# Optimization experiments

Hardware: AMD Instinct MI355X
Metric: run time of the kernel (lower is better)

The kernel has to match this reference:

```python
import jax, jax.numpy as jnp
import numpy as np
import math

DIM = 512      # vMF embedding dim
B = 512        # batch
K = 10         # sample_size
C = 8192       # num_classes
L = 0.7        # kappa_confidence
T_REJ = 32     # fixed rejection-sampling tries (acceptance ~0.7 per try)


def _vmf_logc(k, dim=DIM):
    # Approximate log normalizer from the paper (approximate_logc=True path).
    nm14 = (dim - 1) / 4.0
    nm12 = (dim - 1) / 2.0
    np12 = (dim + 1) / 2.0
    sqrtm = jnp.sqrt(nm12 * nm12 + k * k)
    sqrtp = jnp.sqrt(np12 * np12 + k * k)
    return nm14 * (jnp.log(nm12 + sqrtm) + jnp.log(nm12 + sqrtp)) - 0.5 * (sqrtm + sqrtp)


def _split(params):
    # params layout: [log_probs(1), means(DIM), hidden_ik(1)] (single component).
    means = params[..., 1:1 + DIM]
    hidden_ik = params[..., -1]
    mu = means / jnp.linalg.norm(means, axis=-1, keepdims=True)
    kappa = 1.0 / jnp.exp(hidden_ik)  # positive(x) = exp(x) parametrization
    return mu, kappa


def _vmf_sample(key, mu, kappa, n):
    # Wood's algorithm, vectorized over (b, n) with fixed-count rejection.
    b, d = mu.shape
    kap = kappa[:, None]  # (b,1)
    bb = (-2.0 * kap + jnp.sqrt(4.0 * kap * kap + (d - 1) ** 2)) / (d - 1)
    x0 = (1.0 - bb) / (1.0 + bb)
    cc = kap * x0 + (d - 1) * jnp.log(1.0 - x0 * x0)
    kz, ku, kv = jax.random.split(key, 3)
    z = jax.random.beta(kz, (d - 1) / 2.0, (d - 1) / 2.0, (T_REJ, b, n))
    w = (1.0 - (1.0 + bb) * z) / (1.0 - (1.0 - bb) * z)  # (T,b,n)
    u = jax.random.uniform(ku, (T_REJ, b, n), minval=1e-10)
    acc = kap * w + (d - 1) * jnp.log(1.0 - x0 * w) - cc >= jnp.log(u)
    idx = jnp.argmax(acc, axis=0)  # first accepted try
    w_sel = jnp.take_along_axis(w, idx[None], axis=0)[0]  # (b,n)
    v = jax.random.normal(kv, (b, n, d))
    v = v - jnp.einsum('bnd,bd->bn', v, mu)[..., None] * mu[:, None, :]
    v = v / jnp.linalg.norm(v, axis=-1, keepdims=True)
    sin_t = jnp.sqrt(jnp.clip(1.0 - w_sel * w_sel, 0.0))
    return w_sel[..., None] * mu[:, None, :] + sin_t[..., None] * v  # (b,n,d)


def setup_inputs() -> dict:
    key = jax.random.key(0)
    kp, kw, kl = jax.random.split(key, 3)
    # Input distribution parameters: random means, hidden_ik ~ log(1/kappa) with realistic kappa.
    parameters = jax.random.normal(kp, (B, DIM + 2), dtype=jnp.float32)
    kappa0 = L / (1.0 - L * L) * (DIM - 1) / math.sqrt(DIM)  # ~31
    parameters = parameters.at[:, -1].set(0.1 * parameters[:, -1] - math.log(kappa0))
    # Class weight, built exactly as in __init__ (non-deterministic target).
    means = jax.random.normal(kw, (C, DIM), dtype=jnp.float32) * (L / (1.0 - L * L) * (DIM - 1) / math.sqrt(DIM))
    norm = jnp.linalg.norm(means, axis=-1, keepdims=True)
    hidden_ik = jnp.log(1.0 / norm)  # ipositive = log
    weight = jnp.concatenate([jnp.zeros((C, 1), jnp.float32), means, hidden_ik], axis=-1)
    log_scale = jnp.asarray(2.773, dtype=jnp.float32)
    labels = jax.random.randint(kl, (B,), 0, C)
    return {"parameters": parameters, "weight": weight, "log_scale": log_scale, "labels": labels}


def reference(parameters, weight, log_scale, labels):
    scale = jnp.exp(log_scale)
    mu_x, kappa_x = _split(parameters)   # (b,d), (b,)
    mu_w, kappa_w = _split(weight)       # (c,d), (c,)
    sample = _vmf_sample(jax.random.key(42), mu_x, kappa_x, K)  # (b,K,d)
    sample = sample / jnp.linalg.norm(sample, axis=-1, keepdims=True)
    # logmls(b,k,c): samples have concentration k1=scale; since all means are unit,
    # ||k1*m1 + k2*m2|| = sqrt(k1^2 + k2^2 + 2*k1*k2*cos) -> single GEMM over d.
    cos = jnp.einsum('bkd,cd->bkc', sample, mu_w)
    k1 = scale
    k2 = kappa_w
    kk = jnp.sqrt(k1 * k1 + k2 * k2 + 2.0 * k1 * (k2 * cos))  # (b,K,c)
    logmls = _vmf_logc(k1) + _vmf_logc(k2)[None, None, :] - _vmf_logc(kk)
    neg_logden = jax.scipy.special.logsumexp(logmls, axis=2) - _vmf_logc(scale)  # (b,K)
    neg_lognum = scale * jnp.einsum('bd,bd->b', mu_x, mu_w[labels])
    losses = neg_logden.mean(axis=1) - neg_lognum  # (b,)
    b = parameters.shape[0]
    logits = jnp.zeros((b, C), parameters.dtype).at[jnp.arange(b), labels].set(-losses)
    return logits
```

## Files before the change

kernel.cpp:

```cpp
#include <hip/hip_runtime.h>
#include <stdint.h>

#define DIMD 512
#define BATCH 512
#define KSAMP 10
#define NCLS 8192
#define TREJ 32

typedef __bf16 bf16x8 __attribute__((ext_vector_type(8)));
typedef float f32x4 __attribute__((ext_vector_type(4)));

__device__ inline uint64_t sm64(uint64_t x) {
  x += 0x9E3779B97F4A7C15ull;
  x = (x ^ (x >> 30)) * 0xBF58476D1CE4E5B9ull;
  x = (x ^ (x >> 27)) * 0x94D049BB133111EBull;
  return x ^ (x >> 31);
}
__device__ inline float u01(uint32_t u) {
  return ((float)u + 0.5f) * 2.3283064365386963e-10f;
}
__device__ inline float normal_from(uint64_t r) {
  float u1 = u01((uint32_t)(r >> 32));
  float u2 = u01((uint32_t)r);
  return sqrtf(-2.0f * __logf(u1)) * __cosf(6.28318530718f * u2);
}
__device__ inline float gamma255(uint64_t& ctr) {
  const float dg = 255.1666667f;
  const float cg = 0.02086730f;
  for (int i = 0; i < 16; i++) {
    uint64_t r = sm64(ctr++);
    float x = normal_from(r);
    float t = fmaf(cg, x, 1.0f);
    if (t <= 0.0f) continue;
    float v3 = t * t * t;
    uint64_t r2 = sm64(ctr++);
    float u3 = u01((uint32_t)(r2 >> 32));
    if (__logf(u3) < 0.5f * x * x + dg * (1.0f - v3 + __logf(v3))) return dg * v3;
  }
  return dg;
}
__device__ inline float wave_sum(float v) {
  #pragma unroll
  for (int o = 32; o > 0; o >>= 1) v += __shfl_down(v, o, 64);
  return __shfl(v, 0, 64);
}
__device__ inline float vmf_logc(float k) {
  float k2 = k * k;
  float sm = sqrtf(65280.25f + k2);
  float sp = sqrtf(65792.25f + k2);
  return 127.75f * (logf(255.5f + sm) + logf(255.5f + sp)) - 0.5f * (sm + sp);
}
__device__ inline unsigned short f2bf(float f) {
  uint32_t u = __float_as_uint(f);
  uint32_t r = (u + 0x7FFFu + ((u >> 16) & 1u)) >> 16;
  return (unsigned short)r;
}
__device__ inline float bf2f(unsigned short s) {
  return __uint_as_float(((uint32_t)s) << 16);
}
__device__ inline void async16(const unsigned short* g, unsigned short* l) {
  __builtin_amdgcn_global_load_lds(
      (const __attribute__((address_space(1))) unsigned int*)g,
      (__attribute__((address_space(3))) unsigned int*)l, 16, 0, 0);
}

__global__ __launch_bounds__(256) void prep_w(const float* __restrict__ weight,
                                              const float* __restrict__ lscale,
                                              unsigned short* __restrict__ muWb,
                                              float4* __restrict__ cparams,
                                              float* __restrict__ rowsum,
                                              float4* __restrict__ out4) {
  __shared__ float red[4];
  int c = blockIdx.x, tid = threadIdx.x;
  if (tid < 128) out4[(size_t)c * 128 + tid] = make_float4(0.f, 0.f, 0.f, 0.f);
  if (c < 20) rowsum[c * 256 + tid] = 0.0f;

  const float* wr = weight + (size_t)c * (DIMD + 2) + 1;
  float v0 = wr[tid], v1 = wr[tid + 256];
  float s = wave_sum(v0 * v0 + v1 * v1);
  if ((tid & 63) == 0) red[tid >> 6] = s;
  __syncthreads();
  float tot = red[0] + red[1] + red[2] + red[3];
  float inv = rsqrtf(tot);
  muWb[(size_t)c * DIMD + tid]       = f2bf(v0 * inv);
  muWb[(size_t)c * DIMD + tid + 256] = f2bf(v1 * inv);
  if (tid == 0) {
    float hik = weight[(size_t)c * (DIMD + 2) + DIMD + 1];
    float kw = expf(-hik);
    float k1 = expf(lscale[0]);
    float lcw = vmf_logc(kw);
    float A2 = fmaf(k1, k1, kw * kw);
    float B2 = 2.0f * k1 * kw;
    const float X0 = 0.9238795f, X1 = 0.3826834f;
    float g0 = lcw - vmf_logc(sqrtf(fmaf(B2,  X0, A2)));
    float g1 = lcw - vmf_logc(sqrtf(fmaf(B2,  X1, A2)));
    float g2 = lcw - vmf_logc(sqrtf(fmaf(B2, -X1, A2)));
    float g3 = lcw - vmf_logc(sqrtf(fmaf(B2, -X0, A2)));
    float b0 = 0.25f * (g0 + g1 + g2 + g3);
    float b1 = 0.5f * (X0 * (g0 - g3) + X1 * (g1 - g2));
    float b2 = 0.5f * 0.7071068f * ((g0 + g3) - (g1 + g2));
    float b3 = 0.5f * (X1 * (g0 - g3) - X0 * (g1 - g2));
    const float L2E = 1.4426950409f;
    cparams[c] = make_float4((b0 - b2) * L2E, (b1 - 3.0f * b3) * L2E,
                             (2.0f * b2) * L2E, (4.0f * b3) * L2E);
  }
}

__global__ __launch_bounds__(256) void sample_kernel(const float* __restrict__ params,
                                                     unsigned short* __restrict__ Sb) {
  int wave = threadIdx.x >> 6, lane = threadIdx.x & 63;
  int row = blockIdx.x * 4 + wave;
  int b = row / KSAMP;
  const float* pr = params + (size_t)b * (DIMD + 2) + 1;

  float mu[8];
  float n2 = 0.0f;
  #pragma unroll
  for (int j = 0; j < 8; j++) { mu[j] = pr[j * 64 + lane]; n2 += mu[j] * mu[j]; }
  n2 = wave_sum(n2);
  float invn = rsqrtf(n2);
  #pragma unroll
  for (int j = 0; j < 8; j++) mu[j] *= invn;

  float kap = __expf(-pr[DIMD]);
  float bb = (-2.0f * kap + sqrtf(fmaf(4.0f * kap, kap, 511.0f * 511.0f))) / 511.0f;
  float x0 = (1.0f - bb) / (1.0f + bb);
  float cc = kap * x0 + 511.0f * __logf(1.0f - x0 * x0);

  uint64_t ctr = (((uint64_t)(row + 1)) << 32) | ((uint64_t)lane << 8);
  float g1 = gamma255(ctr);
  float g2 = gamma255(ctr);
  float z = g1 / (g1 + g2);
  float wt = (1.0f - (1.0f + bb) * z) / (1.0f - (1.0f - bb) * z);
  uint64_t r = sm64(ctr++);
  float u = u01((uint32_t)(r >> 32));
  float lhs = kap * wt + 511.0f * __logf(1.0f - x0 * wt) - cc;
  bool acc = (lane < TREJ) && (lhs >= __logf(fmaxf(u, 1e-10f)));
  uint64_t mask = __ballot(acc);
  int sel = mask ? (__ffsll((unsigned long long)mask) - 1) : 0;
  float w = __shfl(wt, sel, 64);

  uint64_t cbase = (((uint64_t)(row + 1)) << 32) | 0x40000000ull;
  float v[8];
  #pragma unroll
  for (int j = 0; j < 8; j++) v[j] = normal_from(sm64(cbase + (uint64_t)(j * 64 + lane)));
  float d = 0.0f;
  #pragma unroll
  for (int j = 0; j < 8; j++) d += v[j] * mu[j];
  d = wave_sum(d);
  float t2 = 0.0f;
  #pragma unroll
  for (int j = 0; j < 8; j++) { v[j] -= d * mu[j]; t2 += v[j] * v[j]; }
  t2 = wave_sum(t2);
  float ivt = rsqrtf(t2);
  float st = sqrtf(fmaxf(0.0f, 1.0f - w * w)) * ivt;
  float sv[8];
  float s2 = 0.0f;
  #pragma unroll
  for (int j = 0; j < 8; j++) { sv[j] = fmaf(st, v[j], w * mu[j]); s2 += sv[j] * sv[j]; }
  s2 = wave_sum(s2);
  float is = rsqrtf(s2);
  #pragma unroll
  for (int j = 0; j < 8; j++) Sb[(size_t)row * DIMD + j * 64 + lane] = f2bf(sv[j] * is);
}

__global__ __launch_bounds__(256, 2) void gemm_lse(const unsigned short* __restrict__ Sb,
                                                   const unsigned short* __restrict__ Wb,
                                                   const float4* __restrict__ cparams,
                                                   float* __restrict__ rowsum) {
  __shared__ __align__(16) unsigned short As[2][256 * 32];
  __shared__ __align__(16) unsigned short Bs[2][128 * 32];
  int tid = threadIdx.x;
  int lane = tid & 63, wave = tid >> 6;
  int tx = lane & 15, tz = lane >> 4;

  int id = blockIdx.x;
  int xcd = id & 7, lid = id >> 3;
  int c0 = (xcd * 8 + (lid & 7)) * 128;
  int r0 = (lid >> 3) * 256;

  int srow = (lane >> 2);
  int kg   = (lane & 3) ^ ((lane >> 3) & 3);
  int chA0 = wave * 4;
  int chB0 = wave * 2;

  f32x4 acc[4][8];
  #pragma unroll
  for (int i = 0; i < 4; i++)
    #pragma unroll
    for (int j = 0; j < 8; j++) acc[i][j] = (f32x4){0.f, 0.f, 0.f, 0.f};

  #pragma unroll
  for (int c = 0; c < 4; c++) {
    int ch = chA0 + c, rowi = ch * 16 + srow;
    async16(&Sb[(size_t)(r0 + rowi) * DIMD + kg * 8], &As[0][ch * 512]);
  }
  #pragma unroll
  for (int c = 0; c < 2; c++) {
    int ch = chB0 + c, rowi = ch * 16 + srow;
    async16(&Wb[(size_t)(c0 + rowi) * DIMD + kg * 8], &Bs[0][ch * 512]);
  }

  int p = 0;
  for (int kt = 0; kt < DIMD; kt += 32) {
    __syncthreads();
    if (kt + 32 < DIMD) {
      #pragma unroll
      for (int c = 0; c < 4; c++) {
        int ch = chA0 + c, rowi = ch * 16 + srow;
        async16(&Sb[(size_t)(r0 + rowi) * DIMD + kt + 32 + kg * 8], &As[p ^ 1][ch * 512]);
      }
      #pragma unroll
      for (int c = 0; c < 2; c++) {
        int ch = chB0 + c, rowi = ch * 16 + srow;
        async16(&Wb[(size_t)(c0 + rowi) * DIMD + kt + 32 + kg * 8], &Bs[p ^ 1][ch * 512]);
      }
    }
    bf16x8 af[4], bf[8];
    int sA = tz ^ ((tx >> 1) & 3);
    #pragma unroll
    for (int mi = 0; mi < 4; mi++) {
      int rA = wave * 64 + mi * 16 + tx;
      af[mi] = *(const bf16x8*)&As[p][rA * 32 + sA * 8];
    }
    #pragma unroll
    for (int ni = 0; ni < 8; ni++) {
      int rB = ni * 16 + tx;
      bf[ni] = *(const bf16x8*)&Bs[p][rB * 32 + sA * 8];
    }
    #pragma unroll
    for (int mi = 0; mi < 4; mi++)
      #pragma unroll
      for (int ni = 0; ni < 8; ni++)
        acc[mi][ni] = __builtin_amdgcn_mfma_f32_16x16x32_bf16(af[mi], bf[ni], acc[mi][ni], 0, 0, 0);
    p ^= 1;
  }

  float4 cp[8];
  #pragma unroll
  for (int ni = 0; ni < 8; ni++) cp[ni] = cparams[c0 + ni * 16 + tx];

  #pragma unroll
  for (int mi = 0; mi < 4; mi++) {
    #pragma unroll
    for (int reg = 0; reg < 4; reg++) {
      float s = 0.0f;
      #pragma unroll
      for (int ni = 0; ni < 8; ni++) {
        float cv = acc[mi][ni][reg];
        float g = fmaf(fmaf(fmaf(cp[ni].w, cv, cp[ni].z), cv, cp[ni].y), cv, cp[ni].x);
        s += exp2f(g);
      }
      #pragma unroll
      for (int o = 1; o < 16; o <<= 1) s += __shfl_xor(s, o, 64);
      if (tx == 0)
        atomicAdd(&rowsum[r0 + wave * 64 + mi * 16 + tz * 4 + reg], s);
    }
  }
}

__global__ __launch_bounds__(64) void finalize_kernel(const float* __restrict__ params,
                                                      const unsigned short* __restrict__ muWb,
                                                      const float* __restrict__ rowsum,
                                                      const int* __restrict__ labels,
                                                      const float* __restrict__ lscale,
                                                      float* __restrict__ out) {
  int b = blockIdx.x;
  int lane = threadIdx.x;
  int lab = labels[b];
  const float* pr = params + (size_t)b * (DIMD + 2) + 1;
  float xv[8];
  float n2 = 0.0f;
  #pragma unroll
  for (int j = 0; j < 8; j++) { xv[j] = pr[j * 64 + lane]; n2 += xv[j] * xv[j]; }
  n2 = wave_sum(n2);
  float invn = rsqrtf(n2);
  float d = 0.0f;
  #pragma unroll
  for (int j = 0; j < 8; j++)
    d += xv[j] * invn * bf2f(muWb[(size_t)lab * DIMD + j * 64 + lane]);
  d = wave_sum(d);
  if (lane == 0) {
    float k1 = expf(lscale[0]);
    float acc = 0.0f;
    #pragma unroll
    for (int k = 0; k < KSAMP; k++) acc += __logf(rowsum[b * KSAMP + k]);
    float loss = acc * (1.0f / KSAMP) - k1 * d;
    out[(size_t)b * NCLS + lab] = -loss;
  }
}

extern "C" void kernel_launch(void* const* d_in, const int* in_sizes, int n_in,
                              void* d_out, int out_size, void* d_ws, size_t ws_size,
                              hipStream_t stream) {
  const float* params = (const float*)d_in[0];
  const float* weight = (const float*)d_in[1];
  const float* lscale = (const float*)d_in[2];
  const int*   labels = (const int*)d_in[3];
  float* out = (float*)d_out;
  char* ws = (char*)d_ws;

  unsigned short* muWb   = (unsigned short*)(ws);
  unsigned short* Sb     = (unsigned short*)(ws + 8388608);
  float4*         cparams= (float4*)(ws + 13631488);
  float*          rowsum = (float*)(ws + 13762560);

  hipLaunchKernelGGL(prep_w, dim3(NCLS), dim3(256), 0, stream,
                     weight, lscale, muWb, cparams, rowsum, (float4*)out);
  hipLaunchKernelGGL(sample_kernel, dim3(BATCH * KSAMP / 4), dim3(256), 0, stream,
                     params, Sb);
  hipLaunchKernelGGL(gemm_lse, dim3((NCLS / 128) * (BATCH * KSAMP / 256)), dim3(256), 0, stream,
                     Sb, muWb, cparams, rowsum);
  hipLaunchKernelGGL(finalize_kernel, dim3(BATCH), dim3(64), 0, stream,
                     params, muWb, rowsum, labels, lscale, out);
}
```

Measured before the change: 168.9 us.

## Switch GEMM operands to FP8 and merge weight prep with sampling kernel

Sample and class-mean vectors are quantized to FP8 (scaled by 16) instead of bf16, and the GEMM uses fp8 MFMA with 64-wide K tiles. The polynomial coefficients are rescaled to absorb the factor of 256. The weight-prep and sampling kernels are fused into one launch, with one wave per class row and the four logc evaluations spread across lanes. Finalize now computes the label dot product in fp32 from the raw weights. This halves operand bandwidth and raises MFMA throughput and cuts a launch, at the cost of FP8 precision in the cosine, which the exponential polynomial amplifies.

```diff
diff --git a/kernel.cpp b/kernel.cpp
--- a/kernel.cpp
+++ b/kernel.cpp
@@ -7,8 +7,8 @@
 #define NCLS 8192
 #define TREJ 32
 
-typedef __bf16 bf16x8 __attribute__((ext_vector_type(8)));
 typedef float f32x4 __attribute__((ext_vector_type(4)));
+typedef long l2 __attribute__((ext_vector_type(2)));
 
 __device__ inline uint64_t sm64(uint64_t x) {
   x += 0x9E3779B97F4A7C15ull;
@@ -50,126 +50,137 @@
   float sp = sqrtf(65792.25f + k2);
   return 127.75f * (logf(255.5f + sm) + logf(255.5f + sp)) - 0.5f * (sm + sp);
 }
-__device__ inline unsigned short f2bf(float f) {
-  uint32_t u = __float_as_uint(f);
-  uint32_t r = (u + 0x7FFFu + ((u >> 16) & 1u)) >> 16;
-  return (unsigned short)r;
-}
-__device__ inline float bf2f(unsigned short s) {
-  return __uint_as_float(((uint32_t)s) << 16);
-}
-__device__ inline void async16(const unsigned short* g, unsigned short* l) {
+__device__ inline void async16(const unsigned char* g, unsigned char* l) {
   __builtin_amdgcn_global_load_lds(
       (const __attribute__((address_space(1))) unsigned int*)g,
       (__attribute__((address_space(3))) unsigned int*)l, 16, 0, 0);
 }
-
-__global__ __launch_bounds__(256) void prep_w(const float* __restrict__ weight,
-                                              const float* __restrict__ lscale,
-                                              unsigned short* __restrict__ muWb,
-                                              float4* __restrict__ cparams,
-                                              float* __restrict__ rowsum,
-                                              float4* __restrict__ out4) {
-  __shared__ float red[4];
-  int c = blockIdx.x, tid = threadIdx.x;
-  if (tid < 128) out4[(size_t)c * 128 + tid] = make_float4(0.f, 0.f, 0.f, 0.f);
-  if (c < 20) rowsum[c * 256 + tid] = 0.0f;
-
-  const float* wr = weight + (size_t)c * (DIMD + 2) + 1;
-  float v0 = wr[tid], v1 = wr[tid + 256];
-  float s = wave_sum(v0 * v0 + v1 * v1);
-  if ((tid & 63) == 0) red[tid >> 6] = s;
-  __syncthreads();
-  float tot = red[0] + red[1] + red[2] + red[3];
-  float inv = rsqrtf(tot);
-  muWb[(size_t)c * DIMD + tid]       = f2bf(v0 * inv);
-  muWb[(size_t)c * DIMD + tid + 256] = f2bf(v1 * inv);
-  if (tid == 0) {
-    float hik = weight[(size_t)c * (DIMD + 2) + DIMD + 1];
+__device__ inline int2 pack_fp8x8(const float* v, float s) {
+  int lo = 0, hi = 0;
+  lo = __builtin_amdgcn_cvt_pk_fp8_f32(v[0] * s, v[1] * s, lo, false);
+  lo = __builtin_amdgcn_cvt_pk_fp8_f32(v[2] * s, v[3] * s, lo, true);
+  hi = __builtin_amdgcn_cvt_pk_fp8_f32(v[4] * s, v[5] * s, hi, false);
+  hi = __builtin_amdgcn_cvt_pk_fp8_f32(v[6] * s, v[7] * s, hi, true);
+  return make_int2(lo, hi);
+}
+__device__ inline int pk_off(int l) {
+  return ((l >> 3) << 6) + ((l & 3) << 4) + (((l & 7) < 4) ? 0 : 8);
+}
+
+__global__ __launch_bounds__(256) void prep_sample(const float* __restrict__ weight,
+                                                   const float* __restrict__ params,
+                                                   const float* __restrict__ lscale,
+                                                   unsigned char* __restrict__ muW8,
+                                                   float4* __restrict__ cparams,
+                                                   float* __restrict__ rowsum,
+                                                   float4* __restrict__ out4,
+                                                   unsigned char* __restrict__ Sb8) {
+  int blk = blockIdx.x, tid = threadIdx.x;
+  int wave = tid >> 6, lane = tid & 63;
+  if (blk < 2048) {
+    out4[(size_t)blk * 512 + tid]       = make_float4(0.f, 0.f, 0.f, 0.f);
+    out4[(size_t)blk * 512 + 256 + tid] = make_float4(0.f, 0.f, 0.f, 0.f);
+    if (blk < 20) rowsum[blk * 256 + tid] = 0.0f;
+
+    int c = blk * 4 + wave;
+    const float* wr = weight + (size_t)c * (DIMD + 2) + 1;
+    float v[8];
+    float n2 = 0.0f;
+    #pragma unroll
+    for (int j = 0; j < 8; j++) { v[j] = wr[lane * 8 + j]; n2 += v[j] * v[j]; }
+    n2 = wave_sum(n2);
+    float inv = rsqrtf(n2) * 16.0f;
+    int2 pk = pack_fp8x8(v, inv);
+    *(int2*)(muW8 + (size_t)c * 512 + pk_off(lane)) = pk;
+
+    float hik = wr[DIMD];
     float kw = expf(-hik);
     float k1 = expf(lscale[0]);
     float lcw = vmf_logc(kw);
     float A2 = fmaf(k1, k1, kw * kw);
     float B2 = 2.0f * k1 * kw;
     const float X0 = 0.9238795f, X1 = 0.3826834f;
-    float g0 = lcw - vmf_logc(sqrtf(fmaf(B2,  X0, A2)));
-    float g1 = lcw - vmf_logc(sqrtf(fmaf(B2,  X1, A2)));
-    float g2 = lcw - vmf_logc(sqrtf(fmaf(B2, -X1, A2)));
-    float g3 = lcw - vmf_logc(sqrtf(fmaf(B2, -X0, A2)));
-    float b0 = 0.25f * (g0 + g1 + g2 + g3);
-    float b1 = 0.5f * (X0 * (g0 - g3) + X1 * (g1 - g2));
-    float b2 = 0.5f * 0.7071068f * ((g0 + g3) - (g1 + g2));
-    float b3 = 0.5f * (X1 * (g0 - g3) - X0 * (g1 - g2));
-    const float L2E = 1.4426950409f;
-    cparams[c] = make_float4((b0 - b2) * L2E, (b1 - 3.0f * b3) * L2E,
-                             (2.0f * b2) * L2E, (4.0f * b3) * L2E);
-  }
-}
-
-__global__ __launch_bounds__(256) void sample_kernel(const float* __restrict__ params,
-                                                     unsigned short* __restrict__ Sb) {
-  int wave = threadIdx.x >> 6, lane = threadIdx.x & 63;
-  int row = blockIdx.x * 4 + wave;
-  int b = row / KSAMP;
-  const float* pr = params + (size_t)b * (DIMD + 2) + 1;
-
-  float mu[8];
-  float n2 = 0.0f;
-  #pragma unroll
-  for (int j = 0; j < 8; j++) { mu[j] = pr[j * 64 + lane]; n2 += mu[j] * mu[j]; }
-  n2 = wave_sum(n2);
-  float invn = rsqrtf(n2);
-  #pragma unroll
-  for (int j = 0; j < 8; j++) mu[j] *= invn;
-
-  float kap = __expf(-pr[DIMD]);
-  float bb = (-2.0f * kap + sqrtf(fmaf(4.0f * kap, kap, 511.0f * 511.0f))) / 511.0f;
-  float x0 = (1.0f - bb) / (1.0f + bb);
-  float cc = kap * x0 + 511.0f * __logf(1.0f - x0 * x0);
-
-  uint64_t ctr = (((uint64_t)(row + 1)) << 32) | ((uint64_t)lane << 8);
-  float g1 = gamma255(ctr);
-  float g2 = gamma255(ctr);
-  float z = g1 / (g1 + g2);
-  float wt = (1.0f - (1.0f + bb) * z) / (1.0f - (1.0f - bb) * z);
-  uint64_t r = sm64(ctr++);
-  float u = u01((uint32_t)(r >> 32));
-  float lhs = kap * wt + 511.0f * __logf(1.0f - x0 * wt) - cc;
-  bool acc = (lane < TREJ) && (lhs >= __logf(fmaxf(u, 1e-10f)));
-  uint64_t mask = __ballot(acc);
-  int sel = mask ? (__ffsll((unsigned long long)mask) - 1) : 0;
-  float w = __shfl(wt, sel, 64);
-
-  uint64_t cbase = (((uint64_t)(row + 1)) << 32) | 0x40000000ull;
-  float v[8];
-  #pragma unroll
-  for (int j = 0; j < 8; j++) v[j] = normal_from(sm64(cbase + (uint64_t)(j * 64 + lane)));
-  float d = 0.0f;
-  #pragma unroll
-  for (int j = 0; j < 8; j++) d += v[j] * mu[j];
-  d = wave_sum(d);
-  float t2 = 0.0f;
-  #pragma unroll
-  for (int j = 0; j < 8; j++) { v[j] -= d * mu[j]; t2 += v[j] * v[j]; }
-  t2 = wave_sum(t2);
-  float ivt = rsqrtf(t2);
-  float st = sqrtf(fmaxf(0.0f, 1.0f - w * w)) * ivt;
-  float sv[8];
-  float s2 = 0.0f;
-  #pragma unroll
-  for (int j = 0; j < 8; j++) { sv[j] = fmaf(st, v[j], w * mu[j]); s2 += sv[j] * sv[j]; }
-  s2 = wave_sum(s2);
-  float is = rsqrtf(s2);
-  #pragma unroll
-  for (int j = 0; j < 8; j++) Sb[(size_t)row * DIMD + j * 64 + lane] = f2bf(sv[j] * is);
-}
-
-__global__ __launch_bounds__(256, 2) void gemm_lse(const unsigned short* __restrict__ Sb,
-                                                   const unsigned short* __restrict__ Wb,
+    int l3 = lane & 3;
+    float Xj = (l3 == 0) ? X0 : (l3 == 1) ? X1 : (l3 == 2) ? -X1 : -X0;
+    float gj = lcw - vmf_logc(sqrtf(fmaf(B2, Xj, A2)));
+    float g0 = __shfl(gj, 0, 64), g1 = __shfl(gj, 1, 64);
+    float g2 = __shfl(gj, 2, 64), g3 = __shfl(gj, 3, 64);
+    if (lane == 0) {
+      float b0 = 0.25f * (g0 + g1 + g2 + g3);
+      float b1 = 0.5f * (X0 * (g0 - g3) + X1 * (g1 - g2));
+      float b2 = 0.5f * 0.7071068f * ((g0 + g3) - (g1 + g2));
+      float b3 = 0.5f * (X1 * (g0 - g3) - X0 * (g1 - g2));
+      const float L2E = 1.4426950409f;
+      const float S1 = 1.0f / 256.0f;
+      float c0f = (b0 - b2) * L2E;
+      float c1f = (b1 - 3.0f * b3) * L2E * S1;
+      float c2f = (2.0f * b2) * L2E * S1 * S1;
+      float c3f = (4.0f * b3) * L2E * S1 * S1 * S1;
+      cparams[c] = make_float4(c0f, c1f, c2f, c3f);
+    }
+  } else {
+    int row = (blk - 2048) * 4 + wave;
+    int b = row / KSAMP;
+    const float* pr = params + (size_t)b * (DIMD + 2) + 1;
+
+    float mu[8];
+    float n2 = 0.0f;
+    #pragma unroll
+    for (int j = 0; j < 8; j++) { mu[j] = pr[lane * 8 + j]; n2 += mu[j] * mu[j]; }
+    n2 = wave_sum(n2);
+    float invn = rsqrtf(n2);
+    #pragma unroll
+    for (int j = 0; j < 8; j++) mu[j] *= invn;
+
+    float kap = __expf(-pr[DIMD]);
+    float bb = (-2.0f * kap + sqrtf(fmaf(4.0f * kap, kap, 511.0f * 511.0f))) / 511.0f;
+    float x0 = (1.0f - bb) / (1.0f + bb);
+    float cc = kap * x0 + 511.0f * __logf(1.0f - x0 * x0);
+
+    uint64_t ctr = (((uint64_t)(row + 1)) << 32) | ((uint64_t)lane << 8);
+    float g1 = gamma255(ctr);
+    float g2 = gamma255(ctr);
+    float z = g1 / (g1 + g2);
+    float wt = (1.0f - (1.0f + bb) * z) / (1.0f - (1.0f - bb) * z);
+    uint64_t r = sm64(ctr++);
+    float u = u01((uint32_t)(r >> 32));
+    float lhs = kap * wt + 511.0f * __logf(1.0f - x0 * wt) - cc;
+    bool acc = (lane < TREJ) && (lhs >= __logf(fmaxf(u, 1e-10f)));
+    uint64_t mask = __ballot(acc);
+    int sel = mask ? (__ffsll((unsigned long long)mask) - 1) : 0;
+    float w = __shfl(wt, sel, 64);
+
+    uint64_t cbase = (((uint64_t)(row + 1)) << 32) | 0x40000000ull;
+    float v[8];
+    #pragma unroll
+    for (int j = 0; j < 8; j++) v[j] = normal_from(sm64(cbase + (uint64_t)(lane * 8 + j)));
+    float d = 0.0f;
+    #pragma unroll
+    for (int j = 0; j < 8; j++) d += v[j] * mu[j];
+    d = wave_sum(d);
+    float t2 = 0.0f;
+    #pragma unroll
+    for (int j = 0; j < 8; j++) { v[j] -= d * mu[j]; t2 += v[j] * v[j]; }
+    t2 = wave_sum(t2);
+    float ivt = rsqrtf(t2);
+    float st = sqrtf(fmaxf(0.0f, 1.0f - w * w)) * ivt;
+    float sv[8];
+    float s2 = 0.0f;
+    #pragma unroll
+    for (int j = 0; j < 8; j++) { sv[j] = fmaf(st, v[j], w * mu[j]); s2 += sv[j] * sv[j]; }
+    s2 = wave_sum(s2);
+    float is = rsqrtf(s2) * 16.0f;
+    int2 pk = pack_fp8x8(sv, is);
+    *(int2*)(Sb8 + (size_t)row * 512 + pk_off(lane)) = pk;
+  }
+}
+
+__global__ __launch_bounds__(256, 2) void gemm_lse(const unsigned char* __restrict__ Sb8,
+                                                   const unsigned char* __restrict__ Wb8,
                                                    const float4* __restrict__ cparams,
                                                    float* __restrict__ rowsum) {
-  __shared__ __align__(16) unsigned short As[2][256 * 32];
-  __shared__ __align__(16) unsigned short Bs[2][128 * 32];
+  __shared__ __align__(16) unsigned char As[2][256 * 64];
+  __shared__ __align__(16) unsigned char Bs[2][128 * 64];
   int tid = threadIdx.x;
   int lane = tid & 63, wave = tid >> 6;
   int tx = lane & 15, tz = lane >> 4;
@@ -193,46 +204,44 @@
   #pragma unroll
   for (int c = 0; c < 4; c++) {
     int ch = chA0 + c, rowi = ch * 16 + srow;
-    async16(&Sb[(size_t)(r0 + rowi) * DIMD + kg * 8], &As[0][ch * 512]);
+    async16(&Sb8[(size_t)(r0 + rowi) * 512 + kg * 16], &As[0][ch * 1024]);
   }
   #pragma unroll
   for (int c = 0; c < 2; c++) {
     int ch = chB0 + c, rowi = ch * 16 + srow;
-    async16(&Wb[(size_t)(c0 + rowi) * DIMD + kg * 8], &Bs[0][ch * 512]);
+    async16(&Wb8[(size_t)(c0 + rowi) * 512 + kg * 16], &Bs[0][ch * 1024]);
   }
 
   int p = 0;
-  for (int kt = 0; kt < DIMD; kt += 32) {
+  for (int kt = 0; kt < 512; kt += 64) {
     __syncthreads();
-    if (kt + 32 < DIMD) {
+    if (kt + 64 < 512) {
       #pragma unroll
       for (int c = 0; c < 4; c++) {
         int ch = chA0 + c, rowi = ch * 16 + srow;
-        async16(&Sb[(size_t)(r0 + rowi) * DIMD + kt + 32 + kg * 8], &As[p ^ 1][ch * 512]);
+        async16(&Sb8[(size_t)(r0 + rowi) * 512 + kt + 64 + kg * 16], &As[p ^ 1][ch * 1024]);
       }
       #pragma unroll
       for (int c = 0; c < 2; c++) {
         int ch = chB0 + c, rowi = ch * 16 + srow;
-        async16(&Wb[(size_t)(c0 + rowi) * DIMD + kt + 32 + kg * 8], &Bs[p ^ 1][ch * 512]);
+        async16(&Wb8[(size_t)(c0 + rowi) * 512 + kt + 64 + kg * 16], &Bs[p ^ 1][ch * 1024]);
       }
     }
-    bf16x8 af[4], bf[8];
+    l2 af[4], bf[8];
     int sA = tz ^ ((tx >> 1) & 3);
     #pragma unroll
-    for (int mi = 0; mi < 4; mi++) {
-      int rA = wave * 64 + mi * 16 + tx;
-      af[mi] = *(const bf16x8*)&As[p][rA * 32 + sA * 8];
-    }
-    #pragma unroll
-    for (int ni = 0; ni < 8; ni++) {
-      int rB = ni * 16 + tx;
-      bf[ni] = *(const bf16x8*)&Bs[p][rB * 32 + sA * 8];
-    }
-    #pragma unroll
     for (int mi = 0; mi < 4; mi++)
-      #pragma unroll
-      for (int ni = 0; ni < 8; ni++)
-        acc[mi][ni] = __builtin_amdgcn_mfma_f32_16x16x32_bf16(af[mi], bf[ni], acc[mi][ni], 0, 0, 0);
+      af[mi] = *(const l2*)&As[p][(wave * 64 + mi * 16 + tx) * 64 + sA * 16];
+    #pragma unroll
+    for (int ni = 0; ni < 8; ni++)
+      bf[ni] = *(const l2*)&Bs[p][(ni * 16 + tx) * 64 + sA * 16];
+    #pragma unroll
+    for (int mi = 0; mi < 4; mi++)
+      #pragma unroll
+      for (int ni = 0; ni < 8; ni++) {
+        acc[mi][ni] = __builtin_amdgcn_mfma_f32_16x16x32_fp8_fp8(af[mi].x, bf[ni].x, acc[mi][ni], 0, 0, 0);
+        acc[mi][ni] = __builtin_amdgcn_mfma_f32_16x16x32_fp8_fp8(af[mi].y, bf[ni].y, acc[mi][ni], 0, 0, 0);
+      }
     p ^= 1;
   }
 
@@ -260,7 +269,7 @@
 }
 
 __global__ __launch_bounds__(64) void finalize_kernel(const float* __restrict__ params,
-                                                      const unsigned short* __restrict__ muWb,
+                                                      const float* __restrict__ weight,
                                                       const float* __restrict__ rowsum,
                                                       const int* __restrict__ labels,
                                                       const float* __restrict__ lscale,
@@ -269,23 +278,21 @@
   int lane = threadIdx.x;
   int lab = labels[b];
   const float* pr = params + (size_t)b * (DIMD + 2) + 1;
-  float xv[8];
-  float n2 = 0.0f;
-  #pragma unroll
-  for (int j = 0; j < 8; j++) { xv[j] = pr[j * 64 + lane]; n2 += xv[j] * xv[j]; }
-  n2 = wave_sum(n2);
-  float invn = rsqrtf(n2);
-  float d = 0.0f;
-  #pragma unroll
-  for (int j = 0; j < 8; j++)
-    d += xv[j] * invn * bf2f(muWb[(size_t)lab * DIMD + j * 64 + lane]);
-  d = wave_sum(d);
+  const float* wr = weight + (size_t)lab * (DIMD + 2) + 1;
+  float nx = 0.0f, nw = 0.0f, d = 0.0f;
+  #pragma unroll
+  for (int j = 0; j < 8; j++) {
+    float xv = pr[j * 64 + lane];
+    float wv = wr[j * 64 + lane];
+    nx += xv * xv; nw += wv * wv; d += xv * wv;
+  }
+  nx = wave_sum(nx); nw = wave_sum(nw); d = wave_sum(d);
   if (lane == 0) {
     float k1 = expf(lscale[0]);
     float acc = 0.0f;
     #pragma unroll
     for (int k = 0; k < KSAMP; k++) acc += __logf(rowsum[b * KSAMP + k]);
-    float loss = acc * (1.0f / KSAMP) - k1 * d;
+    float loss = acc * (1.0f / KSAMP) - k1 * d * rsqrtf(nx) * rsqrtf(nw);
     out[(size_t)b * NCLS + lab] = -loss;
   }
 }
@@ -300,17 +307,15 @@
   float* out = (float*)d_out;
   char* ws = (char*)d_ws;
 
-  unsigned short* muWb   = (unsigned short*)(ws);
-  unsigned short* Sb     = (unsigned short*)(ws + 8388608);
-  float4*         cparams= (float4*)(ws + 13631488);
-  float*          rowsum = (float*)(ws + 13762560);
-
-  hipLaunchKernelGGL(prep_w, dim3(NCLS), dim3(256), 0, stream,
-                     weight, lscale, muWb, cparams, rowsum, (float4*)out);
-  hipLaunchKernelGGL(sample_kernel, dim3(BATCH * KSAMP / 4), dim3(256), 0, stream,
-                     params, Sb);
+  unsigned char* muW8    = (unsigned char*)(ws);
+  unsigned char* Sb8     = (unsigned char*)(ws + 4194304);
+  float4*        cparams = (float4*)(ws + 6815744);
+  float*         rowsum  = (float*)(ws + 6946816);
+
+  hipLaunchKernelGGL(prep_sample, dim3(2048 + BATCH * KSAMP / 4), dim3(256), 0, stream,
+                     weight, params, lscale, muW8, cparams, rowsum, (float4*)out, Sb8);
   hipLaunchKernelGGL(gemm_lse, dim3((NCLS / 128) * (BATCH * KSAMP / 256)), dim3(256), 0, stream,
-                     Sb, muWb, cparams, rowsum);
+                     Sb8, muW8, cparams, rowsum);
   hipLaunchKernelGGL(finalize_kernel, dim3(BATCH), dim3(64), 0, stream,
-                     params, muWb, rowsum, labels, lscale, out);
-}
+                     params, weight, rowsum, labels, lscale, out);
+}
```

New measurement: 141.0 us. 1.2x faster.
